# Kernel optimization log

Hardware: AMD Instinct MI355X
Metric: run time of the kernel (lower is better)

The kernel has to match this reference:

```python
import jax, jax.numpy as jnp
import numpy as np

N = 50000      # nodes
E = 800000     # edges (avg degree 16)
F_IN = 256     # num_node_features
H = 256        # hidden_dim
L = 2          # num_message_passing_rounds - 1 hidden conv layers


def setup_inputs() -> dict:
    key = jax.random.key(0)
    ks = jax.random.split(key, 8)
    x = jax.random.normal(ks[0], (N, F_IN), dtype=jnp.float32)
    edge_index = jax.random.randint(ks[1], (2, E), 0, N, dtype=jnp.int32)
    init = lambda k, shape, fan: jax.random.normal(k, shape, dtype=jnp.float32) / np.float32(np.sqrt(fan))
    WA_in = init(ks[2], (F_IN, H), F_IN)   # proj_in.A weight (stored [in,out])
    WB_in = init(ks[3], (F_IN, H), F_IN)   # proj_in.B weight
    A_stack = init(ks[4], (L, H, H), H)    # conv layers' A weights
    B_stack = init(ks[5], (L, H, H), H)    # conv layers' B weights
    W_out = init(ks[6], (H, 1), H)         # proj_out weight
    b_out = jnp.zeros((1,), jnp.float32)   # proj_out bias
    return {"x": x, "edge_index": edge_index, "WA_in": WA_in, "WB_in": WB_in,
            "A_stack": A_stack, "B_stack": B_stack, "W_out": W_out, "b_out": b_out}


def reference(x, edge_index, WA_in, WB_in, A_stack, B_stack, W_out, b_out):
    src, dst = edge_index[0], edge_index[1]
    # in-degree per node; PyG scatter-mean divides by max(deg, 1)
    deg = jax.ops.segment_sum(jnp.ones((E,), x.dtype), dst, num_segments=N)
    inv_deg = (1.0 / jnp.maximum(deg, 1.0))[:, None]  # [N,1]

    def mean_agg(h):
        # gather x_j = h[src], scatter-mean into dst -> [N, d]
        return jax.ops.segment_sum(h[src], dst, num_segments=N) * inv_deg

    # proj_in: A(mean_msg) + B(x)
    h = mean_agg(x) @ WA_in + x @ WB_in
    # hidden conv rounds with sigmoid (use_relu=False)
    for i in range(L):
        h = jax.nn.sigmoid(mean_agg(h) @ A_stack[i] + h @ B_stack[i])
    # proj_out + squeeze (output_logits=True)
    return (h @ W_out + b_out).squeeze()  # [N]
```

## Files before the change

kernel.cpp:

```cpp
#include <hip/hip_runtime.h>

typedef unsigned short u16;
typedef unsigned int u32;
typedef __attribute__((ext_vector_type(8))) short short8;
typedef __attribute__((ext_vector_type(4))) float f32x4;
typedef __attribute__((ext_vector_type(2))) float f32x2;

__device__ __forceinline__ float bf2f(u16 u) {
    return __uint_as_float(((u32)u) << 16);
}
__device__ __forceinline__ u16 f2bf(float f) {
    u32 u = __float_as_uint(f);
    u += 0x7fff + ((u >> 16) & 1);
    return (u16)(u >> 16);
}
__device__ __forceinline__ u32 pack2(float a, float b) {
    return (u32)f2bf(a) | ((u32)f2bf(b) << 16);
}
__device__ __forceinline__ u32 pk_fp8x4(float f0, float f1, float f2, float f3) {
    int w = __builtin_amdgcn_cvt_pk_fp8_f32(f0, f1, 0, false);
    w = __builtin_amdgcn_cvt_pk_fp8_f32(f2, f3, w, true);
    return (u32)w;
}
__device__ __forceinline__ void acc4(float* a, u32 w) {
    f32x2 lo = __builtin_amdgcn_cvt_pk_f32_fp8((int)w, false);
    f32x2 hi = __builtin_amdgcn_cvt_pk_f32_fp8((int)w, true);
    a[0] += lo.x; a[1] += lo.y; a[2] += hi.x; a[3] += hi.y;
}
__device__ __forceinline__ void acc4m(float* a, u32 w, float m) {
    f32x2 lo = __builtin_amdgcn_cvt_pk_f32_fp8((int)w, false);
    f32x2 hi = __builtin_amdgcn_cvt_pk_f32_fp8((int)w, true);
    a[0] += m * lo.x; a[1] += m * lo.y; a[2] += m * hi.x; a[3] += m * hi.y;
}
__device__ __forceinline__ void acc16(float* a, uint4 v) {
    acc4(a + 0, v.x); acc4(a + 4, v.y); acc4(a + 8, v.z); acc4(a + 12, v.w);
}
__device__ __forceinline__ void acc16m(float* a, uint4 v, float m) {
    acc4m(a + 0, v.x, m); acc4m(a + 4, v.y, m); acc4m(a + 8, v.z, m); acc4m(a + 12, v.w, m);
}


__global__ __launch_bounds__(256) void prep_kernel(const float* __restrict__ x,
                                                   u16* __restrict__ xb, u32* __restrict__ xq,
                                                   int n, int nx,
                                                   const float* __restrict__ WA,
                                                   const float* __restrict__ WB,
                                                   const float* __restrict__ As,
                                                   const float* __restrict__ Bs,
                                                   u16* __restrict__ wT, int nlayers, int nw,
                                                   const int* __restrict__ dst,
                                                   int* __restrict__ ccnt, int e, int nb) {
    __shared__ int h[256];
    int b = blockIdx.x;
    int tid = threadIdx.x;
    if (b < nx) {
        int i = b * 256 + tid;
        int row = i >> 6;
        ushort4 o;
        u32 q;
        if (row < n) {
            float4 v = ((const float4*)x)[i];
            o.x = f2bf(v.x); o.y = f2bf(v.y); o.z = f2bf(v.z); o.w = f2bf(v.w);
            q = pk_fp8x4(v.x, v.y, v.z, v.w);
        } else {
            o.x = o.y = o.z = o.w = 0;
            q = 0;
        }
        ((ushort4*)xb)[i] = o;
        xq[i] = q;
    } else if (b < nx + nw) {
        int i = (b - nx) * 256 + tid;
        const int per = 256 * 512;
        if (i >= nlayers * per) return;
        int l = i / per;
        int rem = i - l * per;
        int nn = rem >> 9;
        int k = rem & 511;
        const float* Aw = (l == 0) ? WA : As + (size_t)(l - 1) * 65536;
        const float* Bw = (l == 0) ? WB : Bs + (size_t)(l - 1) * 65536;
        float v = (k < 256) ? Aw[(size_t)k * 256 + nn] : Bw[(size_t)(k - 256) * 256 + nn];
        wT[i] = f2bf(v);
    } else {
        h[tid] = 0;
        __syncthreads();
        int e0 = (b - nx - nw) * 4096;
#pragma unroll
        for (int j = 0; j < 16; ++j) {
            int i = e0 + j * 256 + tid;
            if (i < e) atomicAdd(&h[dst[i] >> 8], 1);
        }
        __syncthreads();
        if (tid < nb) {
            int v = h[tid];
            if (v) atomicAdd(&ccnt[tid], v);
        }
    }
}


__global__ __launch_bounds__(256) void scan_coarse_kernel(const int* __restrict__ ccnt,
                                                          int* __restrict__ cbase,
                                                          int* __restrict__ rowptr,
                                                          int nb, int n, int e) {
    __shared__ int sh[256];
    int t = threadIdx.x;
    int v = (t < nb) ? ccnt[t] : 0;
    int x = v;
    sh[t] = x; __syncthreads();
    for (int o = 1; o < 256; o <<= 1) {
        int y = (t >= o) ? sh[t - o] : 0;
        __syncthreads();
        x += y; sh[t] = x; __syncthreads();
    }
    if (t < nb) cbase[t] = x - v;
    if (t == 0) { cbase[nb] = e; rowptr[n] = e; }
}

__global__ __launch_bounds__(256) void passA_kernel(const int* __restrict__ src,
                                                    const int* __restrict__ dst,
                                                    const int* __restrict__ cbase,
                                                    int* __restrict__ cfill,
                                                    u32* __restrict__ tmp, int e, int nb) {
    __shared__ int ph[256], pb[256], pr[256], cb[256];
    __shared__ u32 ed[4096];
    int tid = threadIdx.x;
    ph[tid] = 0; pr[tid] = 0;
    cb[tid] = (tid < nb) ? cbase[tid] : 0;
    __syncthreads();
    int e0 = blockIdx.x * 4096;
#pragma unroll
    for (int j = 0; j < 16; ++j) {
        int i = e0 + j * 256 + tid;
        u32 p = 0xFFFFFFFFu;
        if (i < e) {
            int d = dst[i];
            p = ((u32)d << 16) | (u32)src[i];
            atomicAdd(&ph[d >> 8], 1);
        }
        ed[j * 256 + tid] = p;
    }
    __syncthreads();
    pb[tid] = (tid < nb && ph[tid]) ? atomicAdd(&cfill[tid], ph[tid]) : 0;
    __syncthreads();
#pragma unroll
    for (int j = 0; j < 16; ++j) {
        u32 p = ed[j * 256 + tid];
        if (p != 0xFFFFFFFFu) {
            int bk = p >> 24;
            int r = atomicAdd(&pr[bk], 1);
            tmp[cb[bk] + pb[bk] + r] = p;
        }
    }
}

__global__ __launch_bounds__(256) void passB_kernel(const u32* __restrict__ tmp,
                                                    const int* __restrict__ cbase,
                                                    int* __restrict__ rowptr,
                                                    float* __restrict__ invd,
                                                    int* __restrict__ srcs, int n) {
    __shared__ int h[256], loc[256], cnt2[256], sh[256];
    int b = blockIdx.x;
    int tid = threadIdx.x;
    int base = cbase[b];
    int cnt = cbase[b + 1] - base;
    int node0 = b << 8;
    h[tid] = 0; cnt2[tid] = 0;
    __syncthreads();
    for (int i = tid; i < cnt; i += 256)
        atomicAdd(&h[(tmp[base + i] >> 16) & 255], 1);
    __syncthreads();
    int c = h[tid];
    int x = c;
    sh[tid] = x; __syncthreads();
    for (int o = 1; o < 256; o <<= 1) {
        int y = (tid >= o) ? sh[tid - o] : 0;
        __syncthreads();
        x += y; sh[tid] = x; __syncthreads();
    }
    loc[tid] = x - c;
    int node = node0 + tid;
    if (node < n) {
        rowptr[node] = base + x - c;
        invd[node] = 1.0f / (float)(c > 0 ? c : 1);
    }
    __syncthreads();
    for (int i = tid; i < cnt; i += 256) {
        u32 p = tmp[base + i];
        int ln = (p >> 16) & 255;
        int r = atomicAdd(&cnt2[ln], 1);
        srcs[base + loc[ln] + r] = (int)(p & 0xffffu);
    }
}


__global__ __launch_bounds__(256) void agg_kernel(const unsigned char* __restrict__ q,
                                                  u16* __restrict__ mb,
                                                  const int* __restrict__ rowptr,
                                                  const int* __restrict__ srcs,
                                                  const float* __restrict__ invd,
                                                  int n, int npad) {
    int gw = (blockIdx.x * 256 + threadIdx.x) >> 6;
    int lane = threadIdx.x & 63;
    int qd = lane >> 4;
    int fl = lane & 15;
    if (gw >= npad) return;
    u16* orow = mb + (size_t)gw * 256;
    if (gw >= n) {
        if (lane < 16) {
            uint4 z; z.x = z.y = z.z = z.w = 0;
            uint4* p = (uint4*)(orow + lane * 16);
            p[0] = z; p[1] = z;
        }
        return;
    }
    int beg = rowptr[gw], end = rowptr[gw + 1];
    float a[16];
#pragma unroll
    for (int i = 0; i < 16; ++i) a[i] = 0.f;
    for (int base = beg; base < end; base += 64) {
        int cnt = end - base;
        if (cnt > 64) cnt = 64;
        int el = (lane < cnt) ? srcs[base + lane] : 0;
        int t = 0;
        for (; 4 * t + 8 <= cnt; t += 2) {
            int s0 = __shfl(el, 4 * t + qd);
            int s1 = __shfl(el, 4 * t + 4 + qd);
            uint4 v0 = *(const uint4*)(q + (size_t)s0 * 256 + fl * 16);
            uint4 v1 = *(const uint4*)(q + (size_t)s1 * 256 + fl * 16);
            acc16(a, v0);
            acc16(a, v1);
        }
        for (; 4 * t < cnt; ++t) {
            int ei = 4 * t + qd;
            int sj = __shfl(el, ei & 63);
            float m = (ei < cnt) ? 1.0f : 0.0f;
            uint4 v = *(const uint4*)(q + (size_t)sj * 256 + fl * 16);
            acc16m(a, v, m);
        }
    }
#pragma unroll
    for (int i = 0; i < 16; ++i) {
        a[i] += __shfl_xor(a[i], 16);
        a[i] += __shfl_xor(a[i], 32);
    }
    if (lane < 16) {
        float sc = invd[gw];
        uint4 o0, o1;
        o0.x = pack2(a[0] * sc, a[1] * sc);
        o0.y = pack2(a[2] * sc, a[3] * sc);
        o0.z = pack2(a[4] * sc, a[5] * sc);
        o0.w = pack2(a[6] * sc, a[7] * sc);
        o1.x = pack2(a[8] * sc, a[9] * sc);
        o1.y = pack2(a[10] * sc, a[11] * sc);
        o1.z = pack2(a[12] * sc, a[13] * sc);
        o1.w = pack2(a[14] * sc, a[15] * sc);
        uint4* p = (uint4*)(orow + lane * 16);
        p[0] = o0; p[1] = o1;
    }
}


__global__ __launch_bounds__(256, 2) void gemm_kernel(const u16* __restrict__ mA,
                                                      const u16* __restrict__ cur,
                                                      const u16* __restrict__ wT,
                                                      u16* __restrict__ outb,
                                                      unsigned char* __restrict__ hqb,
                                                      const float* __restrict__ wo,
                                                      const float* __restrict__ bo,
                                                      float* __restrict__ out,
                                                      int n, int apply_sigmoid, int fin) {
    __shared__ u16 lA[128 * 32];
    __shared__ u16 lB[256 * 32];
    __shared__ float lO[2][128];
    int r0 = blockIdx.x * 128;
    int tid = threadIdx.x;
    int lane = tid & 63;
    int w = tid >> 6;
    int wrow = w >> 1, wcol = w & 1;
    int lrow = lane & 15, quad = lane >> 4;

    f32x4 acc[4][8] = {};

    for (int ks = 0; ks < 16; ++ks) {
        int k0 = ks * 32;
        const u16* srcA = (k0 < 256) ? mA : cur;
        int kk = k0 & 255;
        __syncthreads();
#pragma unroll
        for (int p = 0; p < 2; ++p) {
            int li = p * 256 + tid;
            int row = li >> 2;
            int seg = (li & 3) << 3;
            const u16* gA = srcA + (size_t)(r0 + row) * 256 + kk + seg;
            __builtin_amdgcn_global_load_lds(
                (__attribute__((address_space(1))) u32*)(gA),
                (__attribute__((address_space(3))) u32*)(lA + (size_t)li * 8), 16, 0, 0);
        }
#pragma unroll
        for (int p = 0; p < 4; ++p) {
            int li = p * 256 + tid;
            int row = li >> 2;
            int seg = (li & 3) << 3;
            const u16* gB = wT + (size_t)row * 512 + k0 + seg;
            __builtin_amdgcn_global_load_lds(
                (__attribute__((address_space(1))) u32*)(gB),
                (__attribute__((address_space(3))) u32*)(lB + (size_t)li * 8), 16, 0, 0);
        }
        __syncthreads();

        short8 a[4], b[8];
#pragma unroll
        for (int t = 0; t < 4; ++t)
            a[t] = *(const short8*)(lA + ((size_t)(wrow * 64 + t * 16 + lrow) * 32 + quad * 8));
#pragma unroll
        for (int t = 0; t < 8; ++t)
            b[t] = *(const short8*)(lB + ((size_t)(wcol * 128 + t * 16 + lrow) * 32 + quad * 8));
#pragma unroll
        for (int rt = 0; rt < 4; ++rt)
#pragma unroll
            for (int ct = 0; ct < 8; ++ct)
                acc[rt][ct] = __builtin_amdgcn_mfma_f32_16x16x32_bf16(a[rt], b[ct], acc[rt][ct], 0, 0, 0);
    }

    if (!fin) {
#pragma unroll
        for (int rt = 0; rt < 4; ++rt) {
            int rbase = r0 + wrow * 64 + rt * 16 + quad * 4;
#pragma unroll
            for (int r = 0; r < 4; ++r) {
                int row = rbase + r;
                if (row < n) {
#pragma unroll
                    for (int ct = 0; ct < 8; ++ct) {
                        float v = acc[rt][ct][r];
                        if (apply_sigmoid) v = 1.0f / (1.0f + __expf(-v));
                        int col = wcol * 128 + ct * 16 + lrow;
                        outb[(size_t)row * 256 + col] = f2bf(v);
                        u32 wq = (u32)__builtin_amdgcn_cvt_pk_fp8_f32(v, v, 0, false);
                        hqb[(size_t)row * 256 + col] = (unsigned char)(wq & 0xff);
                    }
                }
            }
        }
    } else {
        float wv[8];
#pragma unroll
        for (int ct = 0; ct < 8; ++ct) wv[ct] = wo[wcol * 128 + ct * 16 + lrow];
#pragma unroll
        for (int rt = 0; rt < 4; ++rt) {
#pragma unroll
            for (int r = 0; r < 4; ++r) {
                float s = 0.f;
#pragma unroll
                for (int ct = 0; ct < 8; ++ct) {
                    float v = acc[rt][ct][r];
                    v = 1.0f / (1.0f + __expf(-v));
                    s += v * wv[ct];
                }
                s += __shfl_xor(s, 1);
                s += __shfl_xor(s, 2);
                s += __shfl_xor(s, 4);
                s += __shfl_xor(s, 8);
                if (lrow == 0) {
                    int rowlocal = wrow * 64 + rt * 16 + quad * 4 + r;
                    lO[wcol][rowlocal] = s;
                }
            }
        }
        __syncthreads();
        if (tid < 128) {
            int row = r0 + tid;
            if (row < n) out[row] = lO[0][tid] + lO[1][tid] + bo[0];
        }
    }
}


extern "C" void kernel_launch(void* const* d_in, const int* in_sizes, int n_in,
                              void* d_out, int out_size, void* d_ws, size_t ws_size,
                              hipStream_t stream) {
    const float* x  = (const float*)d_in[0];
    const int*   ei = (const int*)d_in[1];
    const float* WA = (const float*)d_in[2];
    const float* WB = (const float*)d_in[3];
    const float* As = (const float*)d_in[4];
    const float* Bs = (const float*)d_in[5];
    const float* Wo = (const float*)d_in[6];
    const float* bo = (const float*)d_in[7];
    float* out = (float*)d_out;

    const int H = 256;
    int N = in_sizes[0] / H;
    int E = in_sizes[1] / 2;
    int L = in_sizes[4] / (H * H);
    int NPAD = (N + 127) & ~127;
    int NB = (N + 255) >> 8;

    char* wsp = (char*)d_ws;
    size_t off = 0;
    auto alloc = [&](size_t b) { size_t o = off; off += (b + 255) & ~(size_t)255; return o; };
    int*   rowptr = (int*)(wsp + alloc((size_t)(NPAD + 1) * 4));
    int*   ccnt   = (int*)(wsp + alloc(2048));
    int*   cfill  = ccnt + 256;
    int*   cbase  = (int*)(wsp + alloc(1032 + 256));
    float* invd   = (float*)(wsp + alloc((size_t)NPAD * 4));
    int*   srcs   = (int*)(wsp + alloc((size_t)E * 4));
    u16*   xb     = (u16*)(wsp + alloc((size_t)NPAD * H * 2));
    u16*   hbuf   = (u16*)(wsp + alloc((size_t)NPAD * H * 2));
    u16*   mb     = (u16*)(wsp + alloc((size_t)NPAD * H * 2));
    u32*   xq     = (u32*)(wsp + alloc((size_t)NPAD * H));
    u32*   hq     = (u32*)(wsp + alloc((size_t)NPAD * H));
    u16*   wT     = (u16*)(wsp + alloc((size_t)(L + 1) * 512 * 256 * 2));
    u32*   tmp    = (u32*)mb;

    const int* esrc = ei;
    const int* edst = ei + E;

    hipMemsetAsync(ccnt, 0, 2048, stream);

    int gridE = (E + 4095) / 4096;
    int nx = NPAD / 4;
    int nw = ((L + 1) * 512 * 256 + 255) / 256;
    prep_kernel<<<nx + nw + gridE, 256, 0, stream>>>(x, xb, xq, N, nx,
                                                     WA, WB, As, Bs, wT, L + 1, nw,
                                                     edst, ccnt, E, NB);
    scan_coarse_kernel<<<1, 256, 0, stream>>>(ccnt, cbase, rowptr, NB, N, E);
    passA_kernel<<<gridE, 256, 0, stream>>>(esrc, edst, cbase, cfill, tmp, E, NB);
    passB_kernel<<<NB, 256, 0, stream>>>(tmp, cbase, rowptr, invd, srcs, N);

    const u16* cur = xb;
    const unsigned char* curq = (const unsigned char*)xq;
    for (int s = 0; s <= L; ++s) {
        int fin = (s == L) ? 1 : 0;
        agg_kernel<<<NPAD / 4, 256, 0, stream>>>(curq, mb, rowptr, srcs, invd, N, NPAD);
        gemm_kernel<<<NPAD / 128, 256, 0, stream>>>(mb, cur, wT + (size_t)s * 512 * 256, hbuf,
                                                    (unsigned char*)hq, Wo, bo, out, N,
                                                    s > 0 ? 1 : 0, fin);
        if (!fin) {
            cur = hbuf;
            curq = (const unsigned char*)hq;
        }
    }
}
```

Measured before the change: 330.9 us.

## Double-buffer GEMM LDS stages and shrink row tile to 64

```diff
diff --git a/kernel.cpp b/kernel.cpp
--- a/kernel.cpp
+++ b/kernel.cpp
@@ -269,72 +269,81 @@
                                                       const float* __restrict__ bo,
                                                       float* __restrict__ out,
                                                       int n, int apply_sigmoid, int fin) {
-    __shared__ u16 lA[128 * 32];
-    __shared__ u16 lB[256 * 32];
-    __shared__ float lO[2][128];
-    int r0 = blockIdx.x * 128;
+    __shared__ u16 lA[2][2][64 * 32];
+    __shared__ u16 lB[2][2][256 * 32];
+    __shared__ float lO[4][64];
+    int r0 = blockIdx.x * 64;
     int tid = threadIdx.x;
     int lane = tid & 63;
     int w = tid >> 6;
-    int wrow = w >> 1, wcol = w & 1;
     int lrow = lane & 15, quad = lane >> 4;
 
-    f32x4 acc[4][8] = {};
-
-    for (int ks = 0; ks < 16; ++ks) {
-        int k0 = ks * 32;
-        const u16* srcA = (k0 < 256) ? mA : cur;
-        int kk = k0 & 255;
-        __syncthreads();
-#pragma unroll
-        for (int p = 0; p < 2; ++p) {
-            int li = p * 256 + tid;
-            int row = li >> 2;
-            int seg = (li & 3) << 3;
-            const u16* gA = srcA + (size_t)(r0 + row) * 256 + kk + seg;
-            __builtin_amdgcn_global_load_lds(
-                (__attribute__((address_space(1))) u32*)(gA),
-                (__attribute__((address_space(3))) u32*)(lA + (size_t)li * 8), 16, 0, 0);
-        }
-#pragma unroll
-        for (int p = 0; p < 4; ++p) {
-            int li = p * 256 + tid;
-            int row = li >> 2;
-            int seg = (li & 3) << 3;
-            const u16* gB = wT + (size_t)row * 512 + k0 + seg;
-            __builtin_amdgcn_global_load_lds(
-                (__attribute__((address_space(1))) u32*)(gB),
-                (__attribute__((address_space(3))) u32*)(lB + (size_t)li * 8), 16, 0, 0);
-        }
-        __syncthreads();
-
-        short8 a[4], b[8];
-#pragma unroll
-        for (int t = 0; t < 4; ++t)
-            a[t] = *(const short8*)(lA + ((size_t)(wrow * 64 + t * 16 + lrow) * 32 + quad * 8));
-#pragma unroll
-        for (int t = 0; t < 8; ++t)
-            b[t] = *(const short8*)(lB + ((size_t)(wcol * 128 + t * 16 + lrow) * 32 + quad * 8));
-#pragma unroll
-        for (int rt = 0; rt < 4; ++rt)
-#pragma unroll
-            for (int ct = 0; ct < 8; ++ct)
-                acc[rt][ct] = __builtin_amdgcn_mfma_f32_16x16x32_bf16(a[rt], b[ct], acc[rt][ct], 0, 0, 0);
+    f32x4 acc[4][4] = {};
+
+    auto STAGE = [&](int buf, int ks) {
+        const u16* srcA = (ks < 4) ? mA : cur;
+        int kk = (ks * 64) & 255;
+#pragma unroll
+        for (int kf = 0; kf < 2; ++kf) {
+            {
+                int li = tid;
+                int row = li >> 2;
+                int seg = (li & 3) << 3;
+                const u16* gA = srcA + (size_t)(r0 + row) * 256 + kk + kf * 32 + seg;
+                __builtin_amdgcn_global_load_lds(
+                    (__attribute__((address_space(1))) u32*)(gA),
+                    (__attribute__((address_space(3))) u32*)(&lA[buf][kf][(size_t)li * 8]), 16, 0, 0);
+            }
+#pragma unroll
+            for (int p = 0; p < 4; ++p) {
+                int li = p * 256 + tid;
+                int row = li >> 2;
+                int seg = (li & 3) << 3;
+                const u16* gB = wT + (size_t)row * 512 + ks * 64 + kf * 32 + seg;
+                __builtin_amdgcn_global_load_lds(
+                    (__attribute__((address_space(1))) u32*)(gB),
+                    (__attribute__((address_space(3))) u32*)(&lB[buf][kf][(size_t)li * 8]), 16, 0, 0);
+            }
+        }
+    };
+
+    STAGE(0, 0);
+    __syncthreads();
+    int buf = 0;
+    for (int ks = 0; ks < 8; ++ks) {
+        if (ks < 7) STAGE(buf ^ 1, ks + 1);
+#pragma unroll
+        for (int kf = 0; kf < 2; ++kf) {
+            short8 a[4], b[4];
+#pragma unroll
+            for (int rt = 0; rt < 4; ++rt)
+                a[rt] = *(const short8*)&lA[buf][kf][(size_t)(rt * 16 + lrow) * 32 + quad * 8];
+#pragma unroll
+            for (int ct = 0; ct < 4; ++ct)
+                b[ct] = *(const short8*)&lB[buf][kf][(size_t)(w * 64 + ct * 16 + lrow) * 32 + quad * 8];
+#pragma unroll
+            for (int rt = 0; rt < 4; ++rt)
+#pragma unroll
+                for (int ct = 0; ct < 4; ++ct)
+                    acc[rt][ct] = __builtin_amdgcn_mfma_f32_16x16x32_bf16(a[rt], b[ct], acc[rt][ct], 0, 0, 0);
+        }
+        __syncthreads();
+        buf ^= 1;
     }
 
     if (!fin) {
 #pragma unroll
         for (int rt = 0; rt < 4; ++rt) {
-            int rbase = r0 + wrow * 64 + rt * 16 + quad * 4;
+            int rbase = r0 + rt * 16 + quad * 4;
 #pragma unroll
             for (int r = 0; r < 4; ++r) {
                 int row = rbase + r;
                 if (row < n) {
 #pragma unroll
-                    for (int ct = 0; ct < 8; ++ct) {
+                    for (int ct = 0; ct < 4; ++ct) {
                         float v = acc[rt][ct][r];
                         if (apply_sigmoid) v = 1.0f / (1.0f + __expf(-v));
-                        int col = wcol * 128 + ct * 16 + lrow;
+                        int col = w * 64 + ct * 16 + lrow;
                         outb[(size_t)row * 256 + col] = f2bf(v);
                         u32 wq = (u32)__builtin_amdgcn_cvt_pk_fp8_f32(v, v, 0, false);
                         hqb[(size_t)row * 256 + col] = (unsigned char)(wq & 0xff);
@@ -343,16 +352,16 @@
             }
         }
     } else {
-        float wv[8];
-#pragma unroll
-        for (int ct = 0; ct < 8; ++ct) wv[ct] = wo[wcol * 128 + ct * 16 + lrow];
+        float wv[4];
+#pragma unroll
+        for (int ct = 0; ct < 4; ++ct) wv[ct] = wo[w * 64 + ct * 16 + lrow];
 #pragma unroll
         for (int rt = 0; rt < 4; ++rt) {
 #pragma unroll
             for (int r = 0; r < 4; ++r) {
                 float s = 0.f;
 #pragma unroll
-                for (int ct = 0; ct < 8; ++ct) {
+                for (int ct = 0; ct < 4; ++ct) {
                     float v = acc[rt][ct][r];
                     v = 1.0f / (1.0f + __expf(-v));
                     s += v * wv[ct];
@@ -362,15 +371,16 @@
                 s += __shfl_xor(s, 4);
                 s += __shfl_xor(s, 8);
                 if (lrow == 0) {
-                    int rowlocal = wrow * 64 + rt * 16 + quad * 4 + r;
-                    lO[wcol][rowlocal] = s;
+                    int rowlocal = rt * 16 + quad * 4 + r;
+                    lO[w][rowlocal] = s;
                 }
             }
         }
         __syncthreads();
-        if (tid < 128) {
+        if (tid < 64) {
             int row = r0 + tid;
-            if (row < n) out[row] = lO[0][tid] + lO[1][tid] + bo[0];
+            if (row < n)
+                out[row] = lO[0][tid] + lO[1][tid] + lO[2][tid] + lO[3][tid] + bo[0];
         }
     }
 }
@@ -433,9 +443,9 @@
     for (int s = 0; s <= L; ++s) {
         int fin = (s == L) ? 1 : 0;
         agg_kernel<<<NPAD / 4, 256, 0, stream>>>(curq, mb, rowptr, srcs, invd, N, NPAD);
-        gemm_kernel<<<NPAD / 128, 256, 0, stream>>>(mb, cur, wT + (size_t)s * 512 * 256, hbuf,
-                                                    (unsigned char*)hq, Wo, bo, out, N,
-                                                    s > 0 ? 1 : 0, fin);
+        gemm_kernel<<<NPAD / 64, 256, 0, stream>>>(mb, cur, wT + (size_t)s * 512 * 256, hbuf,
+                                                   (unsigned char*)hq, Wo, bo, out, N,
+                                                   s > 0 ? 1 : 0, fin);
         if (!fin) {
             cur = hbuf;
             curq = (const unsigned char*)hq;
```

Measured after the change: 400.9 us. 1.21x slower.
